# Kernel optimization log

Hardware: AMD Instinct MI355X
Metric: run time of the kernel (lower is better)

Reference implementation:

```python
import jax, jax.numpy as jnp
import numpy as np

D = 128          # embedding_size
K = 1024         # num_embedding
DECAY = 0.99
EPS = 1e-5
VQ_COMMIT = 0.25
B, T = 16, 4096


def setup_inputs() -> dict:
    key = jax.random.key(0)
    k1, k2, k3 = jax.random.split(key, 3)
    emb = jax.random.normal(k2, (D, K), dtype=jnp.float32)
    return {
        "input": jax.random.normal(k1, (B, T, D), dtype=jnp.float32),
        "embedding": emb,
        "cluster_size": jnp.zeros((K,), dtype=jnp.float32),
        "embedding_mean": emb.copy(),
    }


def reference(input, embedding, cluster_size, embedding_mean):
    # ---- quantize: squared-distance argmin over codebook ----
    flatten = input.reshape(-1, D)                                   # [N, D]
    dist = ((flatten ** 2).sum(1, keepdims=True)
            - 2.0 * flatten @ embedding
            + (embedding ** 2).sum(0, keepdims=True))                # [N, K]
    embedding_ind = jnp.argmin(dist, axis=1)                         # [N]
    code = embedding_ind.reshape(input.shape[:-1])                   # [B, T]

    # ---- dequantize: codebook gather ----
    quantize = jnp.take(embedding.T, code, axis=0)                   # [B, T, D]

    # ---- EMA codebook update (training mode) ----
    N = flatten.shape[0]
    counts = jax.ops.segment_sum(jnp.ones((N,), input.dtype), embedding_ind,
                                 num_segments=K)                     # [K]
    emb_sum = jax.ops.segment_sum(flatten, embedding_ind,
                                  num_segments=K).T                  # [D, K]
    new_cluster_size = cluster_size * DECAY + (1.0 - DECAY) * counts
    new_embedding_mean = embedding_mean * DECAY + (1.0 - DECAY) * emb_sum
    n = new_cluster_size.sum()
    cs = (new_cluster_size + EPS) / (n + K * EPS) * n
    new_embedding = new_embedding_mean / cs[None, :]                 # [D, K]

    # ---- straight-through estimator + commitment loss ----
    quantize_st = input + jax.lax.stop_gradient(quantize - input)
    diff = VQ_COMMIT * jnp.mean(
        (jax.lax.stop_gradient(quantize_st) - input) ** 2)

    return (quantize_st, diff, code,
            new_embedding, new_cluster_size, new_embedding_mean)
```

## Files before the change

kernel.cpp:

```cpp
#include <hip/hip_runtime.h>
#include <hip/hip_fp16.h>
#include <math.h>

#define D_ 128
#define K_ 1024
#define N_ 65536
#define DECAY_ 0.99f
#define OMD_ 0.01f
#define EPS_ 1e-5f
#define VQC_ 0.25f
#define M1_ 0.14f
#define M2_ 0.14f
#define BIAS_ 96.0f
#define CLMIN_ 0.5f
#define CLMAX_ 508.0f
#define WSEG 32

typedef __attribute__((ext_vector_type(8))) _Float16 half8;
typedef __attribute__((ext_vector_type(4))) float f32x4;

#define WOFF_CODE  0
#define WOFF_E2    65536
#define WOFF_CNT   66560
#define WOFF_SSQ   67584
#define WOFF_RCNT  67585
#define WOFF_BASE  67648
#define WOFF_CURS  68736
#define WOFF_ORDER 69760
#define WOFF_ET    136320
#define WOFF_PART  267392
#define WOFF_CSORT 398464
#define WOFF_RLIST 791680
#define WOFF_EF    857216

#define OOFF_Q     0
#define OOFF_DIFF  8388608
#define OOFF_CODE  8388609
#define OOFF_NEMB  8454145
#define OOFF_NCS   8585217
#define OOFF_NMEAN 8586241

__device__ __forceinline__ unsigned umin32(unsigned a, unsigned b) { return a < b ? a : b; }
__device__ __forceinline__ unsigned umax32(unsigned a, unsigned b) { return a > b ? a : b; }

__device__ __forceinline__ void gld16(const unsigned short* g, unsigned short* l) {
    __builtin_amdgcn_global_load_lds(
        (const __attribute__((address_space(1))) unsigned int*)g,
        (__attribute__((address_space(3))) unsigned int*)l, 16, 0, 0);
}

__launch_bounds__(256)
__global__ void k_prep(const float* __restrict__ E, float* __restrict__ Et,
                       unsigned short* __restrict__ Ef, float* __restrict__ e2,
                       int* __restrict__ cnt, int* __restrict__ zc,
                       float* __restrict__ part1) {
    __shared__ float tile[128 * 17];
    __shared__ float e2s[16];
    int tid = threadIdx.x;
    int b = blockIdx.x;
    int c0 = b * 16;
    if (b == 0) {
        for (int i = tid; i < 1026; i += 256) cnt[i] = 0;
    }
    if (b == 1) {
        for (int i = tid; i < 1024; i += 256) zc[i] = 0;
    }
    #pragma unroll
    for (int i = 0; i < 8; ++i) part1[b * 2048 + i * 256 + tid] = 0.f;
    if (tid < 16) e2s[tid] = 0.f;
    #pragma unroll
    for (int i = 0; i < 8; ++i) {
        int idx = i * 256 + tid;
        int d = idx >> 4, cc = idx & 15;
        tile[d * 17 + cc] = E[d * K_ + c0 + cc];
    }
    __syncthreads();
    #pragma unroll
    for (int i = 0; i < 8; ++i) {
        int idx = i * 256 + tid;
        int cc = idx >> 7, d = idx & 127;
        Et[(size_t)(c0 + cc) * D_ + d] = tile[d * 17 + cc];
    }
    int L = tid & 63, s = tid >> 6;
    int cc = L & 15;
    int d0 = s * 32 + ((L >> 4) << 3);
    unsigned short h[8];
    float sq = 0.f;
    #pragma unroll
    for (int j = 0; j < 8; ++j) {
        float e = tile[(d0 + j) * 17 + cc];
        sq = fmaf(e, e, sq);
        h[j] = __half_as_ushort(__float2half(-2.f * e));
    }
    int T = b * 256 + tid;
    #pragma unroll
    for (int j = 0; j < 8; ++j) Ef[T * 8 + j] = h[j];
    atomicAdd(&e2s[cc], sq);
    __syncthreads();
    if (tid < 16) {
        e2[c0 + tid] = e2s[tid];
    }
}

__launch_bounds__(512, 4)
__global__ void k_argmin_mfma(const float* __restrict__ x, const unsigned short* __restrict__ Ef,
                              const float* __restrict__ e2,
                              int* __restrict__ code_i, float* __restrict__ code_f,
                              int* __restrict__ cnt, int* __restrict__ rcnt,
                              int* __restrict__ rlist, const float* __restrict__ Et) {
    __shared__ unsigned short Bs[3][8192];
    __shared__ float e2s[K_];
    int tid = threadIdx.x;
    int w = tid >> 6, L = tid & 63, quad = L >> 4, col = L & 15;
    int mg = w >> 1, ng = w & 1;
    int n0 = blockIdx.x * 128;

    for (int i = tid; i < K_; i += 512) e2s[i] = e2[i];

    half8 ah[2][4];
    #pragma unroll
    for (int mt = 0; mt < 2; ++mt) {
        int tok = n0 + (2 * mg + mt) * 16 + col;
        #pragma unroll
        for (int s = 0; s < 4; ++s) {
            const float* p = x + (size_t)tok * D_ + s * 32 + quad * 8;
            float4 u0 = *(const float4*)(p);
            float4 u1 = *(const float4*)(p + 4);
            ah[mt][s][0] = (_Float16)u0.x; ah[mt][s][1] = (_Float16)u0.y;
            ah[mt][s][2] = (_Float16)u0.z; ah[mt][s][3] = (_Float16)u0.w;
            ah[mt][s][4] = (_Float16)u1.x; ah[mt][s][5] = (_Float16)u1.y;
            ah[mt][s][6] = (_Float16)u1.z; ah[mt][s][7] = (_Float16)u1.w;
        }
    }

    unsigned k1[2][4], k2[2][4], k3[2][4];
    #pragma unroll
    for (int mt = 0; mt < 2; ++mt)
        #pragma unroll
        for (int r = 0; r < 4; ++r) {
            k1[mt][r] = 0xFFFFFFFFu; k2[mt][r] = 0xFFFFFFFFu; k3[mt][r] = 0xFFFFFFFFu;
        }

    __syncthreads();

    #pragma unroll
    for (int i = 0; i < 2; ++i) {
        int o = (w * 2 + i) * 512;
        gld16(Ef + o + L * 8, &Bs[0][o]);
    }
    #pragma unroll
    for (int i = 0; i < 2; ++i) {
        int o = (w * 2 + i) * 512;
        gld16(Ef + 8192 + o + L * 8, &Bs[1][o]);
    }

    #pragma unroll
    for (int q = 0; q < 16; ++q) {
        if (q < 15) asm volatile("s_waitcnt vmcnt(2)" ::: "memory");
        else        asm volatile("s_waitcnt vmcnt(0)" ::: "memory");
        __builtin_amdgcn_s_barrier();
        asm volatile("" ::: "memory");

        const unsigned short* Bp = &Bs[q % 3][0];

        float evb[2];
        #pragma unroll
        for (int nn = 0; nn < 2; ++nn)
            evb[nn] = e2s[q * 64 + (2 * ng + nn) * 16 + col] + BIAS_;
        f32x4 acc[2][2];
        #pragma unroll
        for (int mt = 0; mt < 2; ++mt)
            #pragma unroll
            for (int nn = 0; nn < 2; ++nn)
                #pragma unroll
                for (int r = 0; r < 4; ++r)
                    acc[mt][nn][r] = evb[nn];

        #pragma unroll
        for (int s = 0; s < 4; ++s) {
            half8 bh[2];
            #pragma unroll
            for (int nn = 0; nn < 2; ++nn) {
                int off = (((2 * ng + nn) * 4 + s) * 64 + L) * 8;
                bh[nn] = *(const half8*)(Bp + off);
            }
            #pragma unroll
            for (int nn = 0; nn < 2; ++nn)
                #pragma unroll
                for (int mt = 0; mt < 2; ++mt)
                    acc[mt][nn] = __builtin_amdgcn_mfma_f32_16x16x32_f16(ah[mt][s], bh[nn], acc[mt][nn], 0, 0, 0);
        }

        #pragma unroll
        for (int nn = 0; nn < 2; ++nn) {
            unsigned cb = (unsigned)(q * 64 + (2 * ng + nn) * 16 + col);
            #pragma unroll
            for (int mt = 0; mt < 2; ++mt)
                #pragma unroll
                for (int r = 0; r < 4; ++r) {
                    float dc = fminf(fmaxf(acc[mt][nn][r], CLMIN_), CLMAX_);
                    unsigned key = (__float_as_uint(dc) & 0xFFFFFC00u) | cb;
                    unsigned m1 = umax32(k1[mt][r], key);
                    k1[mt][r]   = umin32(k1[mt][r], key);
                    unsigned m2 = umax32(k2[mt][r], m1);
                    k2[mt][r]   = umin32(k2[mt][r], m1);
                    k3[mt][r]   = umin32(k3[mt][r], m2);
                }
        }

        if (q < 14) {
            const unsigned short* src = Ef + (q + 2) * 8192;
            int sl = (q + 2) % 3;
            #pragma unroll
            for (int i = 0; i < 2; ++i) {
                int o = (w * 2 + i) * 512;
                gld16(src + o + L * 8, &Bs[sl][o]);
            }
        }
    }

    __syncthreads();
    unsigned* mk1 = (unsigned*)&Bs[0][0];
    unsigned* mk2 = mk1 + 256;
    unsigned* mk3 = mk2 + 256;

    #pragma unroll
    for (int mt = 0; mt < 2; ++mt) {
        #pragma unroll
        for (int r = 0; r < 4; ++r) {
            unsigned a = k1[mt][r], b = k2[mt][r], c = k3[mt][r];
            #pragma unroll
            for (int m = 1; m < 16; m <<= 1) {
                unsigned ao = (unsigned)__shfl_xor((int)a, m);
                unsigned bo = (unsigned)__shfl_xor((int)b, m);
                unsigned co = (unsigned)__shfl_xor((int)c, m);
                unsigned t1 = umax32(a, ao);
                a           = umin32(a, ao);
                unsigned s2 = umin32(b, bo);
                unsigned u  = umax32(t1, s2);
                b           = umin32(t1, s2);
                c           = umin32(u, umin32(c, co));
            }
            if (col == 0) {
                int tl = (2 * mg + mt) * 16 + quad * 4 + r;
                mk1[tl * 2 + ng] = a;
                mk2[tl * 2 + ng] = b;
                mk3[tl * 2 + ng] = c;
            }
        }
    }
    __syncthreads();
    if (tid < 128) {
        unsigned a1 = mk1[tid * 2], b1 = mk1[tid * 2 + 1];
        unsigned a2 = mk2[tid * 2], b2 = mk2[tid * 2 + 1];
        unsigned a3 = mk3[tid * 2], b3 = mk3[tid * 2 + 1];
        unsigned t1 = umax32(a1, b1);
        unsigned kk1 = umin32(a1, b1);
        unsigned s2 = umin32(a2, b2);
        unsigned kk2 = umin32(t1, s2);
        unsigned u  = umax32(t1, s2);
        unsigned kk3 = umin32(u, umin32(a3, b3));

        int i1 = (int)(kk1 & 1023u), i2 = (int)(kk2 & 1023u);
        float d1 = __uint_as_float(kk1 & 0xFFFFFC00u);
        float d2 = __uint_as_float(kk2 & 0xFFFFFC00u);
        float d3 = __uint_as_float(kk3 & 0xFFFFFC00u);
        int tok = n0 + tid;

        if (d3 - d1 < M2_) {
            code_i[tok] = i1;
            code_f[tok] = (float)i1;
            atomicAdd(cnt + i1, 1);
            int p = atomicAdd(rcnt, 1);
            rlist[p] = tok;
        } else {
            int win = i1;
            if (d2 - d1 < M1_) {
                const float* xr = x  + (size_t)tok * D_;
                const float* ea = Et + (size_t)i1 * D_;
                const float* eb = Et + (size_t)i2 * D_;
                float s1 = 0.f, sB = 0.f;
                #pragma unroll 4
                for (int dd = 0; dd < D_; dd += 4) {
                    float4 xv = *(const float4*)(xr + dd);
                    float4 av = *(const float4*)(ea + dd);
                    float4 bv = *(const float4*)(eb + dd);
                    s1 = fmaf(xv.x, av.x, s1); s1 = fmaf(xv.y, av.y, s1);
                    s1 = fmaf(xv.z, av.z, s1); s1 = fmaf(xv.w, av.w, s1);
                    sB = fmaf(xv.x, bv.x, sB); sB = fmaf(xv.y, bv.y, sB);
                    sB = fmaf(xv.z, bv.z, sB); sB = fmaf(xv.w, bv.w, sB);
                }
                float ex1 = e2s[i1] - 2.f * s1;
                float ex2 = e2s[i2] - 2.f * sB;
                if (ex2 < ex1 || (ex2 == ex1 && i2 < i1)) win = i2;
            }
            code_i[tok] = win;
            code_f[tok] = (float)win;
            atomicAdd(cnt + win, 1);
        }
    }
}

__launch_bounds__(256)
__global__ void k_fix(const float* __restrict__ x, const float* __restrict__ Et,
                      const float* __restrict__ e2, const int* __restrict__ rcnt,
                      const int* __restrict__ rlist, int* __restrict__ code_i,
                      float* __restrict__ code_f, int* __restrict__ cnt) {
    __shared__ float4 xs[32];
    __shared__ float  e2s[K_];
    __shared__ float  sd[8];
    __shared__ int    si[8];
    int tid = threadIdx.x;
    int lane = tid & 63, w = tid >> 6;
    int half = lane >> 5;
    int q32  = lane & 31;
    int slot = w * 2 + half;
    int nr = *rcnt;
    for (int i = tid; i < K_; i += 256) e2s[i] = e2[i];

    for (int it = blockIdx.x; it < nr; it += gridDim.x) {
        __syncthreads();
        int tok = rlist[it];
        if (tid < 32) xs[tid] = ((const float4*)(x + (size_t)tok * D_))[tid];
        __syncthreads();
        float4 xv = xs[q32];
        float bd = INFINITY; int bb = 0;
        for (int c0 = 0; c0 < K_; c0 += 32) {
            int ca = c0 + slot, cb = ca + 8, cc = ca + 16, cd = ca + 24;
            float4 ea = ((const float4*)(Et + (size_t)ca * D_))[q32];
            float4 eb = ((const float4*)(Et + (size_t)cb * D_))[q32];
            float4 ec = ((const float4*)(Et + (size_t)cc * D_))[q32];
            float4 ed = ((const float4*)(Et + (size_t)cd * D_))[q32];
            float da = xv.x * ea.x + xv.y * ea.y + xv.z * ea.z + xv.w * ea.w;
            float db = xv.x * eb.x + xv.y * eb.y + xv.z * eb.z + xv.w * eb.w;
            float dc = xv.x * ec.x + xv.y * ec.y + xv.z * ec.z + xv.w * ec.w;
            float dd = xv.x * ed.x + xv.y * ed.y + xv.z * ed.z + xv.w * ed.w;
            #pragma unroll
            for (int m = 1; m <= 16; m <<= 1) {
                da += __shfl_xor(da, m);
                db += __shfl_xor(db, m);
                dc += __shfl_xor(dc, m);
                dd += __shfl_xor(dd, m);
            }
            float A = e2s[ca] - 2.f * da;
            float B = e2s[cb] - 2.f * db;
            float C = e2s[cc] - 2.f * dc;
            float Dv = e2s[cd] - 2.f * dd;
            if (A  < bd) { bd = A;  bb = ca; }
            if (B  < bd) { bd = B;  bb = cb; }
            if (C  < bd) { bd = C;  bb = cc; }
            if (Dv < bd) { bd = Dv; bb = cd; }
        }
        if (q32 == 0) { sd[slot] = bd; si[slot] = bb; }
        __syncthreads();
        if (tid == 0) {
            float fb = sd[0]; int fi = si[0];
            #pragma unroll
            for (int s = 1; s < 8; ++s) {
                if (sd[s] < fb || (sd[s] == fb && si[s] < fi)) { fb = sd[s]; fi = si[s]; }
            }
            int ob = code_i[tok];
            if (fi != ob) {
                code_i[tok] = fi;
                code_f[tok] = (float)fi;
                atomicAdd(cnt + ob, -1);
                atomicAdd(cnt + fi, 1);
            }
        }
    }
}

__launch_bounds__(256)
__global__ void k_scatter(const int* __restrict__ cnt, const int* __restrict__ code_i,
                          int* __restrict__ zc, int* __restrict__ order,
                          int* __restrict__ csort) {
    __shared__ int sbase[1024];
    __shared__ int wtot[4];
    int t = threadIdx.x;
    int lane = t & 63, wv = t >> 6;
    int c4[4];
    #pragma unroll
    for (int j = 0; j < 4; ++j) c4[j] = cnt[4 * t + j];
    int s = c4[0] + c4[1] + c4[2] + c4[3];
    int ps = s;
    #pragma unroll
    for (int m = 1; m < 64; m <<= 1) {
        int o = __shfl_up(ps, m);
        if (lane >= m) ps += o;
    }
    if (lane == 63) wtot[wv] = ps;
    __syncthreads();
    int woff = 0;
    for (int i = 0; i < 4; ++i) if (i < wv) woff += wtot[i];
    int run = woff + ps - s;
    #pragma unroll
    for (int j = 0; j < 4; ++j) {
        sbase[4 * t + j] = run;
        run += c4[j];
    }
    __syncthreads();

    int n = blockIdx.x * 256 + t;
    int c = code_i[n];
    int pos = sbase[c] + atomicAdd(zc + c, 1);
    order[pos] = n;
    csort[pos] = c;
}

__launch_bounds__(256)
__global__ void k_segdeq(const float* __restrict__ x, const float* __restrict__ Et,
                         const int* __restrict__ order, const int* __restrict__ csort,
                         float* __restrict__ part1, float* __restrict__ outq,
                         float* __restrict__ ssqp) {
    __shared__ int sn[WSEG], sc[WSEG];
    __shared__ float wsum[4];
    int tid = threadIdx.x;
    int d = tid & 127;
    int h = tid >> 7;
    int i0 = blockIdx.x * WSEG;
    if (tid < WSEG) { sn[tid] = order[i0 + tid]; sc[tid] = csort[i0 + tid]; }
    __syncthreads();
    int s0 = h * 16;
    int cprev = sc[s0];
    float eq = Et[(size_t)cprev * D_ + d];
    float acc = 0.f, ssql = 0.f;
    float xv = x[(size_t)sn[s0] * D_ + d];
    #pragma unroll 4
    for (int j = 0; j < 16; ++j) {
        int sj = s0 + j;
        float xn = (j < 15) ? x[(size_t)sn[sj + 1] * D_ + d] : 0.f;
        int c = sc[sj];
        if (c != cprev) {
            atomicAdd(&part1[(size_t)cprev * D_ + d], acc);
            acc = 0.f;
            eq = Et[(size_t)c * D_ + d];
            cprev = c;
        }
        float qv = xv + (eq - xv);
        outq[(size_t)sn[sj] * D_ + d] = qv;
        float t = qv - xv;
        ssql = fmaf(t, t, ssql);
        acc += xv;
        xv = xn;
    }
    atomicAdd(&part1[(size_t)cprev * D_ + d], acc);

    #pragma unroll
    for (int off = 32; off > 0; off >>= 1) ssql += __shfl_down(ssql, off);
    if ((tid & 63) == 0) wsum[tid >> 6] = ssql;
    __syncthreads();
    if (tid == 0) atomicAdd(ssqp, (wsum[0] + wsum[1]) + (wsum[2] + wsum[3]));
}

__launch_bounds__(256)
__global__ void k_embed(const float* __restrict__ em, const float* __restrict__ part1,
                        const int* __restrict__ cnt, const float* __restrict__ csz,
                        const float* __restrict__ ssqp, float* __restrict__ out_nmean,
                        float* __restrict__ out_nemb, float* __restrict__ out_ncs,
                        float* __restrict__ out_diff) {
    int tid = threadIdx.x;
    __shared__ float red[256];

    float ls = 0.f;
    for (int j = tid; j < K_; j += 256) ls += csz[j] * DECAY_ + OMD_ * (float)cnt[j];
    red[tid] = ls;
    __syncthreads();
    for (int off = 128; off > 0; off >>= 1) {
        if (tid < off) red[tid] += red[tid + off];
        __syncthreads();
    }
    float n = red[0];
    __syncthreads();

    if (blockIdx.x == 0) {
        for (int j = tid; j < K_; j += 256)
            out_ncs[j] = csz[j] * DECAY_ + OMD_ * (float)cnt[j];
        if (tid == 0) *out_diff = VQC_ * ssqp[0] / (float)(N_ * D_);
    }

    int i = blockIdx.x * 256 + tid;
    int k = i & (K_ - 1);
    int d = i >> 10;
    float ncs_k = csz[k] * DECAY_ + OMD_ * (float)cnt[k];
    float csk = (ncs_k + EPS_) / (n + (float)K_ * EPS_) * n;
    float es = part1[(size_t)k * D_ + d];
    float nm = em[i] * DECAY_ + OMD_ * es;
    out_nmean[i] = nm;
    out_nemb[i]  = nm / csk;
}

extern "C" void kernel_launch(void* const* d_in, const int* in_sizes, int n_in,
                              void* d_out, int out_size, void* d_ws, size_t ws_size,
                              hipStream_t stream) {
    const float* x   = (const float*)d_in[0];
    const float* E   = (const float*)d_in[1];
    const float* csz = (const float*)d_in[2];
    const float* em  = (const float*)d_in[3];
    float* out = (float*)d_out;
    float* W   = (float*)d_ws;

    int*   code_i = (int*)(W + WOFF_CODE);
    float* e2     = W + WOFF_E2;
    int*   cnt    = (int*)(W + WOFF_CNT);
    float* ssqp   = W + WOFF_SSQ;
    int*   rcnt   = (int*)(W + WOFF_RCNT);
    int*   zc     = (int*)(W + WOFF_CURS);
    int*   order  = (int*)(W + WOFF_ORDER);
    float* Et     = W + WOFF_ET;
    float* part1  = W + WOFF_PART;
    int*   csort  = (int*)(W + WOFF_CSORT);
    int*   rlist  = (int*)(W + WOFF_RLIST);
    unsigned short* Ef = (unsigned short*)(W + WOFF_EF);

    k_prep<<<64, 256, 0, stream>>>(E, Et, Ef, e2, cnt, zc, part1);
    k_argmin_mfma<<<N_ / 128, 512, 0, stream>>>(x, Ef, e2, code_i,
                                                out + OOFF_CODE, cnt, rcnt, rlist, Et);
    k_fix<<<2048, 256, 0, stream>>>(x, Et, e2, rcnt, rlist, code_i, out + OOFF_CODE, cnt);
    k_scatter<<<N_ / 256, 256, 0, stream>>>(cnt, code_i, zc, order, csort);
    k_segdeq<<<N_ / WSEG, 256, 0, stream>>>(x, Et, order, csort, part1,
                                            out + OOFF_Q, ssqp);
    k_embed<<<(D_ * K_) / 256, 256, 0, stream>>>(em, part1, cnt, csz, ssqp,
                                                 out + OOFF_NMEAN, out + OOFF_NEMB,
                                                 out + OOFF_NCS, out + OOFF_DIFF);
}
```

Baseline: 223.0 us.

## Fuse dequantize and commitment-loss into argmin kernel, patch changed codes in fix

```diff
diff --git a/kernel.cpp b/kernel.cpp
--- a/kernel.cpp
+++ b/kernel.cpp
@@ -107,9 +107,11 @@
                               const float* __restrict__ e2,
                               int* __restrict__ code_i, float* __restrict__ code_f,
                               int* __restrict__ cnt, int* __restrict__ rcnt,
-                              int* __restrict__ rlist, const float* __restrict__ Et) {
+                              int* __restrict__ rlist, const float* __restrict__ Et,
+                              float* __restrict__ outq, float* __restrict__ ssqp) {
     __shared__ unsigned short Bs[3][8192];
     __shared__ float e2s[K_];
+    __shared__ float ws[8];
     int tid = threadIdx.x;
     int w = tid >> 6, L = tid & 63, quad = L >> 4, col = L & 15;
     int mg = w >> 1, ng = w & 1;
@@ -223,6 +225,7 @@
     unsigned* mk1 = (unsigned*)&Bs[0][0];
     unsigned* mk2 = mk1 + 256;
     unsigned* mk3 = mk2 + 256;
+    int* codeL    = (int*)(mk3 + 256);
 
     #pragma unroll
     for (int mt = 0; mt < 2; ++mt) {
@@ -270,6 +273,7 @@
         if (d3 - d1 < M2_) {
             code_i[tok] = i1;
             code_f[tok] = (float)i1;
+            codeL[tid] = i1;
             atomicAdd(cnt + i1, 1);
             int p = atomicAdd(rcnt, 1);
             rlist[p] = tok;
@@ -296,7 +300,44 @@
             }
             code_i[tok] = win;
             code_f[tok] = (float)win;
+            codeL[tid] = win;
             atomicAdd(cnt + win, 1);
+        }
+    }
+    __syncthreads();
+
+    {
+        int tk = tid >> 2;
+        int db = (tid & 3) * 32;
+        int tok = n0 + tk;
+        int c = codeL[tk];
+        const float* xr = x   + (size_t)tok * D_ + db;
+        const float* er = Et  + (size_t)c   * D_ + db;
+        float*       qr = outq + (size_t)tok * D_ + db;
+        float ssql = 0.f;
+        #pragma unroll
+        for (int k2 = 0; k2 < 8; ++k2) {
+            float4 xv = *(const float4*)(xr + k2 * 4);
+            float4 ev = *(const float4*)(er + k2 * 4);
+            float4 qv;
+            qv.x = xv.x + (ev.x - xv.x);
+            qv.y = xv.y + (ev.y - xv.y);
+            qv.z = xv.z + (ev.z - xv.z);
+            qv.w = xv.w + (ev.w - xv.w);
+            *(float4*)(qr + k2 * 4) = qv;
+            float t0 = qv.x - xv.x, t1 = qv.y - xv.y;
+            float t2 = qv.z - xv.z, t3 = qv.w - xv.w;
+            ssql += t0 * t0 + t1 * t1 + t2 * t2 + t3 * t3;
+        }
+        #pragma unroll
+        for (int off = 32; off > 0; off >>= 1) ssql += __shfl_down(ssql, off);
+        if ((tid & 63) == 0) ws[tid >> 6] = ssql;
+        __syncthreads();
+        if (tid == 0) {
+            float s = 0.f;
+            #pragma unroll
+            for (int i = 0; i < 8; ++i) s += ws[i];
+            atomicAdd(ssqp, s);
         }
     }
 }
@@ -305,11 +346,14 @@
 __global__ void k_fix(const float* __restrict__ x, const float* __restrict__ Et,
                       const float* __restrict__ e2, const int* __restrict__ rcnt,
                       const int* __restrict__ rlist, int* __restrict__ code_i,
-                      float* __restrict__ code_f, int* __restrict__ cnt) {
+                      float* __restrict__ code_f, int* __restrict__ cnt,
+                      float* __restrict__ outq, float* __restrict__ ssqp) {
     __shared__ float4 xs[32];
     __shared__ float  e2s[K_];
     __shared__ float  sd[8];
     __shared__ int    si[8];
+    __shared__ int    sfi, sob, schg;
+    __shared__ float  wsf[4];
     int tid = threadIdx.x;
     int lane = tid & 63, w = tid >> 6;
     int half = lane >> 5;
@@ -360,12 +404,32 @@
                 if (sd[s] < fb || (sd[s] == fb && si[s] < fi)) { fb = sd[s]; fi = si[s]; }
             }
             int ob = code_i[tok];
+            sfi = fi; sob = ob; schg = (fi != ob);
             if (fi != ob) {
                 code_i[tok] = fi;
                 code_f[tok] = (float)fi;
                 atomicAdd(cnt + ob, -1);
                 atomicAdd(cnt + fi, 1);
             }
+        }
+        __syncthreads();
+        if (schg) {
+            float dl = 0.f;
+            if (tid < 128) {
+                float xd = ((const float*)xs)[tid];
+                float eo = Et[(size_t)sob * D_ + tid];
+                float en = Et[(size_t)sfi * D_ + tid];
+                float qo = xd + (eo - xd);
+                float qn = xd + (en - xd);
+                outq[(size_t)tok * D_ + tid] = qn;
+                float to_ = qo - xd, tn_ = qn - xd;
+                dl = tn_ * tn_ - to_ * to_;
+            }
+            #pragma unroll
+            for (int off = 32; off > 0; off >>= 1) dl += __shfl_down(dl, off);
+            if ((tid & 63) == 0) wsf[tid >> 6] = dl;
+            __syncthreads();
+            if (tid == 0) atomicAdd(ssqp, (wsf[0] + wsf[1]) + (wsf[2] + wsf[3]));
         }
     }
 }
@@ -408,12 +472,9 @@
 }
 
 __launch_bounds__(256)
-__global__ void k_segdeq(const float* __restrict__ x, const float* __restrict__ Et,
-                         const int* __restrict__ order, const int* __restrict__ csort,
-                         float* __restrict__ part1, float* __restrict__ outq,
-                         float* __restrict__ ssqp) {
+__global__ void k_segsum(const float* __restrict__ x, const int* __restrict__ order,
+                         const int* __restrict__ csort, float* __restrict__ part1) {
     __shared__ int sn[WSEG], sc[WSEG];
-    __shared__ float wsum[4];
     int tid = threadIdx.x;
     int d = tid & 127;
     int h = tid >> 7;
@@ -422,8 +483,7 @@
     __syncthreads();
     int s0 = h * 16;
     int cprev = sc[s0];
-    float eq = Et[(size_t)cprev * D_ + d];
-    float acc = 0.f, ssql = 0.f;
+    float acc = 0.f;
     float xv = x[(size_t)sn[s0] * D_ + d];
     #pragma unroll 4
     for (int j = 0; j < 16; ++j) {
@@ -433,23 +493,12 @@
         if (c != cprev) {
             atomicAdd(&part1[(size_t)cprev * D_ + d], acc);
             acc = 0.f;
-            eq = Et[(size_t)c * D_ + d];
             cprev = c;
         }
-        float qv = xv + (eq - xv);
-        outq[(size_t)sn[sj] * D_ + d] = qv;
-        float t = qv - xv;
-        ssql = fmaf(t, t, ssql);
         acc += xv;
         xv = xn;
     }
     atomicAdd(&part1[(size_t)cprev * D_ + d], acc);
-
-    #pragma unroll
-    for (int off = 32; off > 0; off >>= 1) ssql += __shfl_down(ssql, off);
-    if ((tid & 63) == 0) wsum[tid >> 6] = ssql;
-    __syncthreads();
-    if (tid == 0) atomicAdd(ssqp, (wsum[0] + wsum[1]) + (wsum[2] + wsum[3]));
 }
 
 __launch_bounds__(256)
@@ -514,11 +563,12 @@
 
     k_prep<<<64, 256, 0, stream>>>(E, Et, Ef, e2, cnt, zc, part1);
     k_argmin_mfma<<<N_ / 128, 512, 0, stream>>>(x, Ef, e2, code_i,
-                                                out + OOFF_CODE, cnt, rcnt, rlist, Et);
-    k_fix<<<2048, 256, 0, stream>>>(x, Et, e2, rcnt, rlist, code_i, out + OOFF_CODE, cnt);
+                                                out + OOFF_CODE, cnt, rcnt, rlist, Et,
+                                                out + OOFF_Q, ssqp);
+    k_fix<<<2048, 256, 0, stream>>>(x, Et, e2, rcnt, rlist, code_i, out + OOFF_CODE,
+                                    cnt, out + OOFF_Q, ssqp);
     k_scatter<<<N_ / 256, 256, 0, stream>>>(cnt, code_i, zc, order, csort);
-    k_segdeq<<<N_ / WSEG, 256, 0, stream>>>(x, Et, order, csort, part1,
-                                            out + OOFF_Q, ssqp);
+    k_segsum<<<N_ / WSEG, 256, 0, stream>>>(x, order, csort, part1);
     k_embed<<<(D_ * K_) / 256, 256, 0, stream>>>(em, part1, cnt, csz, ssqp,
                                                  out + OOFF_NMEAN, out + OOFF_NEMB,
                                                  out + OOFF_NCS, out + OOFF_DIFF);
```

Result: faster. 210.2 us (-5.7%).

## Move dequantize write and loss sum into scatter kernel with coalesced token order

Applied to the files above, without the earlier changes.

```diff
diff --git a/kernel.cpp b/kernel.cpp
--- a/kernel.cpp
+++ b/kernel.cpp
@@ -373,9 +373,13 @@
 __launch_bounds__(256)
 __global__ void k_scatter(const int* __restrict__ cnt, const int* __restrict__ code_i,
                           int* __restrict__ zc, int* __restrict__ order,
-                          int* __restrict__ csort) {
+                          int* __restrict__ csort, const float* __restrict__ x,
+                          const float* __restrict__ Et, float* __restrict__ outq,
+                          float* __restrict__ ssqp) {
     __shared__ int sbase[1024];
     __shared__ int wtot[4];
+    __shared__ int scode[256];
+    __shared__ float wsf[4];
     int t = threadIdx.x;
     int lane = t & 63, wv = t >> 6;
     int c4[4];
@@ -402,18 +406,49 @@
 
     int n = blockIdx.x * 256 + t;
     int c = code_i[n];
+    scode[t] = c;
     int pos = sbase[c] + atomicAdd(zc + c, 1);
     order[pos] = n;
     csort[pos] = c;
+    __syncthreads();
+
+    int tk8 = t >> 3;
+    int db  = (t & 7) * 16;
+    float ssql = 0.f;
+    #pragma unroll
+    for (int pass = 0; pass < 8; ++pass) {
+        int li  = pass * 32 + tk8;
+        int tok = blockIdx.x * 256 + li;
+        int cc  = scode[li];
+        const float* xr = x    + (size_t)tok * D_ + db;
+        const float* er = Et   + (size_t)cc  * D_ + db;
+        float*       qr = outq + (size_t)tok * D_ + db;
+        #pragma unroll
+        for (int k2 = 0; k2 < 4; ++k2) {
+            float4 xv = *(const float4*)(xr + k2 * 4);
+            float4 ev = *(const float4*)(er + k2 * 4);
+            float4 qv;
+            qv.x = xv.x + (ev.x - xv.x);
+            qv.y = xv.y + (ev.y - xv.y);
+            qv.z = xv.z + (ev.z - xv.z);
+            qv.w = xv.w + (ev.w - xv.w);
+            *(float4*)(qr + k2 * 4) = qv;
+            float t0 = qv.x - xv.x, t1 = qv.y - xv.y;
+            float t2 = qv.z - xv.z, t3 = qv.w - xv.w;
+            ssql += t0 * t0 + t1 * t1 + t2 * t2 + t3 * t3;
+        }
+    }
+    #pragma unroll
+    for (int off = 32; off > 0; off >>= 1) ssql += __shfl_down(ssql, off);
+    if ((t & 63) == 0) wsf[t >> 6] = ssql;
+    __syncthreads();
+    if (t == 0) atomicAdd(ssqp, (wsf[0] + wsf[1]) + (wsf[2] + wsf[3]));
 }
 
 __launch_bounds__(256)
-__global__ void k_segdeq(const float* __restrict__ x, const float* __restrict__ Et,
-                         const int* __restrict__ order, const int* __restrict__ csort,
-                         float* __restrict__ part1, float* __restrict__ outq,
-                         float* __restrict__ ssqp) {
+__global__ void k_segsum(const float* __restrict__ x, const int* __restrict__ order,
+                         const int* __restrict__ csort, float* __restrict__ part1) {
     __shared__ int sn[WSEG], sc[WSEG];
-    __shared__ float wsum[4];
     int tid = threadIdx.x;
     int d = tid & 127;
     int h = tid >> 7;
@@ -422,8 +457,7 @@
     __syncthreads();
     int s0 = h * 16;
     int cprev = sc[s0];
-    float eq = Et[(size_t)cprev * D_ + d];
-    float acc = 0.f, ssql = 0.f;
+    float acc = 0.f;
     float xv = x[(size_t)sn[s0] * D_ + d];
     #pragma unroll 4
     for (int j = 0; j < 16; ++j) {
@@ -433,23 +467,12 @@
         if (c != cprev) {
             atomicAdd(&part1[(size_t)cprev * D_ + d], acc);
             acc = 0.f;
-            eq = Et[(size_t)c * D_ + d];
             cprev = c;
         }
-        float qv = xv + (eq - xv);
-        outq[(size_t)sn[sj] * D_ + d] = qv;
-        float t = qv - xv;
-        ssql = fmaf(t, t, ssql);
         acc += xv;
         xv = xn;
     }
     atomicAdd(&part1[(size_t)cprev * D_ + d], acc);
-
-    #pragma unroll
-    for (int off = 32; off > 0; off >>= 1) ssql += __shfl_down(ssql, off);
-    if ((tid & 63) == 0) wsum[tid >> 6] = ssql;
-    __syncthreads();
-    if (tid == 0) atomicAdd(ssqp, (wsum[0] + wsum[1]) + (wsum[2] + wsum[3]));
 }
 
 __launch_bounds__(256)
@@ -516,9 +539,9 @@
     k_argmin_mfma<<<N_ / 128, 512, 0, stream>>>(x, Ef, e2, code_i,
                                                 out + OOFF_CODE, cnt, rcnt, rlist, Et);
     k_fix<<<2048, 256, 0, stream>>>(x, Et, e2, rcnt, rlist, code_i, out + OOFF_CODE, cnt);
-    k_scatter<<<N_ / 256, 256, 0, stream>>>(cnt, code_i, zc, order, csort);
-    k_segdeq<<<N_ / WSEG, 256, 0, stream>>>(x, Et, order, csort, part1,
-                                            out + OOFF_Q, ssqp);
+    k_scatter<<<N_ / 256, 256, 0, stream>>>(cnt, code_i, zc, order, csort,
+                                            x, Et, out + OOFF_Q, ssqp);
+    k_segsum<<<N_ / WSEG, 256, 0, stream>>>(x, order, csort, part1);
     k_embed<<<(D_ * K_) / 256, 256, 0, stream>>>(em, part1, cnt, csz, ssqp,
                                                  out + OOFF_NMEAN, out + OOFF_NEMB,
                                                  out + OOFF_NCS, out + OOFF_DIFF);
```

Result: faster. 206.7 us (-7.3%).
